# Optimization experiments

Measured on AMD Instinct MI355X. Metric: run time of the kernel, lower is better.

Reference implementation:

```python
import jax, jax.numpy as jnp
import numpy as np

L = 2        # n_layers
D = 128      # embed_dim
H = 4        # n_heads
HD = D // H  # head_dim
B = 2
N = 4096
PERIOD = 2.0
WINDOW = 0.5
EPS = 1e-5
NF = D // 4  # n_frequencies = embed_dim / (n_dimensions * 2), n_dimensions=2


def setup_inputs() -> dict:
    key = jax.random.key(0)
    ks = jax.random.split(key, 12)
    s = 0.05  # weight init scale
    inp = {
        'x': jax.random.normal(ks[0], (B, N, D), jnp.float32),
        'pos': jax.random.uniform(ks[1], (B, N, 2), jnp.float32),
        'Wq_w': jax.random.normal(ks[2], (L, D, D), jnp.float32) * s,
        'Wq_b': jnp.zeros((L, D), jnp.float32),
        'Wk_w': jax.random.normal(ks[3], (L, D, D), jnp.float32) * s,
        'Wk_b': jnp.zeros((L, D), jnp.float32),
        'Wv_w': jax.random.normal(ks[4], (L, D, D), jnp.float32) * s,
        'Wv_b': jnp.zeros((L, D), jnp.float32),
        'Wo_w': jax.random.normal(ks[5], (L, D, D), jnp.float32) * s,
        'Wo_b': jnp.zeros((L, D), jnp.float32),
        'n1_g': jnp.ones((L, D), jnp.float32),
        'n1_b': jnp.zeros((L, D), jnp.float32),
        'n2_g': jnp.ones((L, D), jnp.float32),
        'n2_b': jnp.zeros((L, D), jnp.float32),
        'l1_w': jax.random.normal(ks[6], (L, D, 2 * D), jnp.float32) * s,
        'l1_b': jnp.zeros((L, 2 * D), jnp.float32),
        'l2_w': jax.random.normal(ks[7], (L, 2 * D, D), jnp.float32) * s,
        'l2_b': jnp.zeros((L, D), jnp.float32),
    }
    return inp


def _batchnorm(x, g, b):
    # BatchNorm1d in training mode over flattened (B*N, D)
    Bb, Nn, Dd = x.shape
    x2 = x.reshape(Bb * Nn, Dd)
    mu = x2.mean(0)
    var = x2.var(0)
    y = (x2 - mu) * jax.lax.rsqrt(var + EPS) * g + b
    return y.reshape(Bb, Nn, Dd)


def _rope(x, pos, freqs):
    # x: (B,N,D), pos: (B,N,2), freqs: (NF,)
    angle = pos[..., None] * freqs            # (B,N,2,NF)
    angle = jnp.repeat(angle, 2, axis=-1)     # (B,N,2,2*NF)
    angle = angle.reshape(x.shape)            # (B,N,D)
    xp = x.reshape(*x.shape[:-1], D // 2, 2)
    x_sw = jnp.stack([-xp[..., 1], xp[..., 0]], axis=-1).reshape(x.shape)
    return jnp.cos(angle) * x + jnp.sin(angle) * x_sw


def _forward(x, pos, Wq_w, Wq_b, Wk_w, Wk_b, Wv_w, Wv_b, Wo_w, Wo_b,
             n1_g, n1_b, n2_g, n2_b, l1_w, l1_b, l2_w, l2_b):
    freqs = 2 * jnp.pi * jnp.arange(1, NF + 1, dtype=x.dtype) / PERIOD
    # window mask: dist(i,j) <= WINDOW/2  -> compare squared distances
    sq = jnp.sum(pos * pos, axis=-1)                          # (B,N)
    d2 = sq[:, :, None] + sq[:, None, :] - 2 * jnp.einsum('bnd,bmd->bnm', pos, pos)
    mask = (d2 <= (WINDOW / 2) ** 2)[:, None, :, :]           # (B,1,N,N)
    scale = 1.0 / jnp.sqrt(jnp.asarray(HD, x.dtype))

    for i in range(L):
        xn = _batchnorm(x, n1_g[i], n1_b[i])
        q = xn @ Wq_w[i] + Wq_b[i]
        k = xn @ Wk_w[i] + Wk_b[i]
        v = xn @ Wv_w[i] + Wv_b[i]
        if i == 0:  # rotary encoding applied at first layer only
            q = _rope(q, pos, freqs)
            k = _rope(k, pos, freqs)
        # split heads: (B,N,D) -> (B,H,N,HD)
        qh = q.reshape(B, N, H, HD).transpose(0, 2, 1, 3)
        kh = k.reshape(B, N, H, HD).transpose(0, 2, 1, 3)
        vh = v.reshape(B, N, H, HD).transpose(0, 2, 1, 3)
        scores = jnp.einsum('bhnd,bhmd->bhnm', qh, kh) * scale
        scores = jnp.where(mask, scores, jnp.finfo(x.dtype).min)
        attn = jax.nn.softmax(scores, axis=-1)
        oh = jnp.einsum('bhnm,bhmd->bhnd', attn, vh)
        o = oh.transpose(0, 2, 1, 3).reshape(B, N, D)
        x = x + (o @ Wo_w[i] + Wo_b[i])
        # FFN block
        xn2 = _batchnorm(x, n2_g[i], n2_b[i])
        h = jax.nn.relu(xn2 @ l1_w[i] + l1_b[i])
        x = x + (h @ l2_w[i] + l2_b[i])
    return x


def reference(x, pos, Wq_w, Wq_b, Wk_w, Wk_b, Wv_w, Wv_b, Wo_w, Wo_b,
              n1_g, n1_b, n2_g, n2_b, l1_w, l1_b, l2_w, l2_b):
    return _forward(x, pos, Wq_w, Wq_b, Wk_w, Wk_b, Wv_w, Wv_b, Wo_w, Wo_b,
                    n1_g, n1_b, n2_g, n2_b, l1_w, l1_b, l2_w, l2_b)
```

## Files before the change

kernel.cpp:

```cpp
#include <hip/hip_runtime.h>
#include <hip/hip_bf16.h>
#include <math.h>

#define LYR 2
#define DIM 128
#define NH 4
#define HD 32
#define BB 2
#define NN 4096
#define MROWS (BB * NN)
#define R2 0.0625f
#define BN_EPS 1e-5f
#define CLOG2E 0.25503594f

typedef __attribute__((ext_vector_type(4))) float f32x4;
typedef __attribute__((ext_vector_type(8))) short bf16x8;
typedef __attribute__((ext_vector_type(4))) short bf16x4;

static __device__ inline unsigned short f2bf(float f) {
  union { float f; unsigned u; } v; v.f = f;
  unsigned r = v.u + 0x7FFFu + ((v.u >> 16) & 1u);
  return (unsigned short)(r >> 16);
}

static __device__ inline float exp2_fast(float x) {
#if defined(__has_builtin)
#if __has_builtin(__builtin_amdgcn_exp2f)
  return __builtin_amdgcn_exp2f(x);
#else
  return exp2f(x);
#endif
#else
  return exp2f(x);
#endif
}

static __device__ inline unsigned cvt_pk_bf16(float lo, float hi) {
  unsigned r;
  asm volatile("v_cvt_pk_bf16_f32 %0, %1, %2" : "=v"(r) : "v"(lo), "v"(hi));
  return r;
}

__global__ __launch_bounds__(256) void wprep_k(const float* __restrict__ Wq,
                                               const float* __restrict__ Wk,
                                               const float* __restrict__ Wv,
                                               const float* __restrict__ Wo,
                                               const float* __restrict__ L1,
                                               const float* __restrict__ L2,
                                               const float* __restrict__ Wqb,
                                               const float* __restrict__ Wkb,
                                               const float* __restrict__ Wvb,
                                               short* __restrict__ wT,
                                               float* __restrict__ qkvb) {
  const int id = blockIdx.x;
  const int l = id >> 7, r = id & 127;
  const size_t lbase = (size_t)l * 131072;
  const float* src; short* dst; int K, N, tk, tn;
  float mult = 1.0f;
  if (r < 64) {
    const int m = r >> 4, tile = r & 15;
    if (m == 0)      { src = Wq + (size_t)l * 16384; mult = CLOG2E; }
    else if (m == 1) src = Wk + (size_t)l * 16384;
    else if (m == 2) src = Wv + (size_t)l * 16384;
    else             src = Wo + (size_t)l * 16384;
    dst = wT + lbase + (size_t)m * 16384;
    K = 128; N = 128; tk = tile >> 2; tn = tile & 3;
  } else if (r < 96) {
    const int tile = r - 64;
    src = L1 + (size_t)l * 32768; dst = wT + lbase + 65536;
    K = 128; N = 256; tk = tile >> 3; tn = tile & 7;
  } else {
    const int tile = r - 96;
    src = L2 + (size_t)l * 32768; dst = wT + lbase + 98304;
    K = 256; N = 128; tk = tile >> 2; tn = tile & 3;
  }
  __shared__ float tl[32][33];
  const int t = threadIdx.x;
  const int rr = t >> 3, c4 = (t & 7) * 4;
  float4 vv = *(const float4*)(src + (size_t)(tk * 32 + rr) * N + tn * 32 + c4);
  tl[rr][c4 + 0] = vv.x; tl[rr][c4 + 1] = vv.y;
  tl[rr][c4 + 2] = vv.z; tl[rr][c4 + 3] = vv.w;
  __syncthreads();
  bf16x4 o4;
  o4[0] = (short)f2bf(tl[c4 + 0][rr] * mult);
  o4[1] = (short)f2bf(tl[c4 + 1][rr] * mult);
  o4[2] = (short)f2bf(tl[c4 + 2][rr] * mult);
  o4[3] = (short)f2bf(tl[c4 + 3][rr] * mult);
  *(bf16x4*)(dst + (size_t)(tn * 32 + rr) * K + tk * 32 + c4) = o4;
  if (r == 0) {
    for (int i = t; i < 384; i += 256) {
      float bv;
      if (i < 128)      bv = Wqb[l * 128 + i] * CLOG2E;
      else if (i < 256) bv = Wkb[l * 128 + i - 128];
      else              bv = Wvb[l * 128 + i - 256];
      qkvb[l * 384 + i] = bv;
    }
  }
}

__global__ __launch_bounds__(256) void copy_stats_k(const float* __restrict__ x,
                                                    float* __restrict__ out,
                                                    float* __restrict__ sums) {
  __shared__ float ss[8][128], sq[8][128];
  const int t = threadIdx.x;
  const int c4 = (t & 31) * 4, rg = t >> 5;
  const size_t base = (size_t)blockIdx.x * (32 * DIM);
  float s0 = 0.f, s1 = 0.f, s2 = 0.f, s3 = 0.f;
  float q0 = 0.f, q1 = 0.f, q2 = 0.f, q3 = 0.f;
  for (int r = rg; r < 32; r += 8) {
    float4 v = *(const float4*)&x[base + (size_t)r * DIM + c4];
    *(float4*)&out[base + (size_t)r * DIM + c4] = v;
    s0 += v.x; q0 += v.x * v.x;
    s1 += v.y; q1 += v.y * v.y;
    s2 += v.z; q2 += v.z * v.z;
    s3 += v.w; q3 += v.w * v.w;
  }
  ss[rg][c4 + 0] = s0; sq[rg][c4 + 0] = q0;
  ss[rg][c4 + 1] = s1; sq[rg][c4 + 1] = q1;
  ss[rg][c4 + 2] = s2; sq[rg][c4 + 2] = q2;
  ss[rg][c4 + 3] = s3; sq[rg][c4 + 3] = q3;
  __syncthreads();
  if (t < 128) {
    float S = 0.f, Q = 0.f;
#pragma unroll
    for (int r2 = 0; r2 < 8; r2++) { S += ss[r2][t]; Q += sq[r2][t]; }
    atomicAdd(&sums[t], S);
    atomicAdd(&sums[128 + t], Q);
  }
}

__global__ __launch_bounds__(256) void bn_apply_k(const float* __restrict__ x,
                                                  const float* __restrict__ sums,
                                                  const float* __restrict__ g,
                                                  const float* __restrict__ bta,
                                                  short* __restrict__ y) {
  const int i4 = blockIdx.x * 256 + threadIdx.x;
  const int dd = (i4 * 4) & (DIM - 1);
  const float inv = 1.0f / (float)MROWS;
  float4 xv = *(const float4*)&x[(size_t)i4 * 4];
  float4 sm = *(const float4*)&sums[dd];
  float4 sq = *(const float4*)&sums[128 + dd];
  float4 gg = *(const float4*)&g[dd];
  float4 bb = *(const float4*)&bta[dd];
  float mu0 = sm.x * inv, mu1 = sm.y * inv, mu2 = sm.z * inv, mu3 = sm.w * inv;
  bf16x4 o;
  o[0] = (short)f2bf((xv.x - mu0) * rsqrtf(sq.x * inv - mu0 * mu0 + BN_EPS) * gg.x + bb.x);
  o[1] = (short)f2bf((xv.y - mu1) * rsqrtf(sq.y * inv - mu1 * mu1 + BN_EPS) * gg.y + bb.y);
  o[2] = (short)f2bf((xv.z - mu2) * rsqrtf(sq.z * inv - mu2 * mu2 + BN_EPS) * gg.z + bb.z);
  o[3] = (short)f2bf((xv.w - mu3) * rsqrtf(sq.w * inv - mu3 * mu3 + BN_EPS) * gg.w + bb.w);
  *(bf16x4*)&y[(size_t)i4 * 4] = o;
}

template <int MODE, bool RELU>
__global__ __launch_bounds__(256) void gemm_bf_k(const short* __restrict__ A,
                                                 const short* __restrict__ WT,
                                                 const float* __restrict__ bias,
                                                 const float* res,
                                                 float* Cf,
                                                 short* __restrict__ Cb,
                                                 float* __restrict__ statsums,
                                                 int K) {
  __shared__ short a_s[64 * 80];
  __shared__ short w_s[64 * 80];
  const int t = threadIdx.x, w = t >> 6, lane = t & 63, g = lane >> 4, i16 = lane & 15;
  const int bm = blockIdx.x * 64, bn = blockIdx.y * 64;
  const int sr = t >> 2, sc = (t & 3) * 8;
  const size_t MN = (size_t)MROWS * DIM;
  f32x4 acc[4];
#pragma unroll
  for (int ct = 0; ct < 4; ct++) acc[ct] = (f32x4){0.f, 0.f, 0.f, 0.f};
  for (int k0 = 0; k0 < K; k0 += 64) {
    __syncthreads();
    *(bf16x8*)&a_s[sr * 80 + sc]      = *(const bf16x8*)(A + (size_t)(bm + sr) * K + k0 + sc);
    *(bf16x8*)&a_s[sr * 80 + sc + 32] = *(const bf16x8*)(A + (size_t)(bm + sr) * K + k0 + sc + 32);
    *(bf16x8*)&w_s[sr * 80 + sc]      = *(const bf16x8*)(WT + (size_t)(bn + sr) * K + k0 + sc);
    *(bf16x8*)&w_s[sr * 80 + sc + 32] = *(const bf16x8*)(WT + (size_t)(bn + sr) * K + k0 + sc + 32);
    __syncthreads();
#pragma unroll
    for (int ks = 0; ks < 2; ks++) {
      bf16x8 af = *(const bf16x8*)&a_s[(16 * w + i16) * 80 + ks * 32 + 8 * g];
#pragma unroll
      for (int ct = 0; ct < 4; ct++) {
        bf16x8 wf = *(const bf16x8*)&w_s[(ct * 16 + i16) * 80 + ks * 32 + 8 * g];
        acc[ct] = __builtin_amdgcn_mfma_f32_16x16x32_bf16(af, wf, acc[ct], 0, 0, 0);
      }
    }
  }
  float s_acc[4], q_acc[4];
#pragma unroll
  for (int ct = 0; ct < 4; ct++) {
    const int col = bn + ct * 16 + i16;
    const float bv = bias[col];
    if (MODE == 3) {
      const int row0 = bm + 16 * w + 4 * g;
      if (col < 256) {
        short* dstb = (col < 128) ? Cb : (Cb + MN);
        const int cc = col & 127;
#pragma unroll
        for (int r = 0; r < 4; r++)
          dstb[(size_t)(row0 + r) * DIM + cc] = (short)f2bf(acc[ct][r] + bv);
      } else {
        const int b_ = row0 >> 12, n_ = row0 & (NN - 1);
        const int hh = (col - 256) >> 5, dd = (col - 256) & 31;
        bf16x4 o4;
#pragma unroll
        for (int r = 0; r < 4; r++) o4[r] = (short)f2bf(acc[ct][r] + bv);
        *(bf16x4*)(Cb + 2 * MN + ((size_t)(b_ * NH + hh) * HD + dd) * NN + n_) = o4;
      }
    } else if (MODE == 0) {
      float ssum = 0.f, qsum = 0.f;
#pragma unroll
      for (int r = 0; r < 4; r++) {
        const int row = bm + 16 * w + 4 * g + r;
        float vv = acc[ct][r] + bv + res[(size_t)row * DIM + col];
        Cf[(size_t)row * DIM + col] = vv;
        ssum += vv; qsum += vv * vv;
      }
      s_acc[ct] = ssum; q_acc[ct] = qsum;
    } else {
#pragma unroll
      for (int r = 0; r < 4; r++) {
        const int row = bm + 16 * w + 4 * g + r;
        float vv = acc[ct][r] + bv;
        if (RELU) vv = fmaxf(vv, 0.f);
        Cb[(size_t)row * (size_t)256 + col] = (short)f2bf(vv);
      }
    }
  }
  if (MODE == 0) {
#pragma unroll
    for (int ct = 0; ct < 4; ct++) {
      s_acc[ct] += __shfl_xor(s_acc[ct], 16, 64);
      s_acc[ct] += __shfl_xor(s_acc[ct], 32, 64);
      q_acc[ct] += __shfl_xor(q_acc[ct], 16, 64);
      q_acc[ct] += __shfl_xor(q_acc[ct], 32, 64);
    }
    float* bs = (float*)a_s;
    __syncthreads();
    if (t < 128) bs[t] = 0.f;
    __syncthreads();
    if (lane < 16) {
#pragma unroll
      for (int ct = 0; ct < 4; ct++) {
        atomicAdd(&bs[ct * 16 + i16], s_acc[ct]);
        atomicAdd(&bs[64 + ct * 16 + i16], q_acc[ct]);
      }
    }
    __syncthreads();
    if (t < 64) {
      atomicAdd(&statsums[bn + t], bs[t]);
      atomicAdd(&statsums[128 + bn + t], bs[64 + t]);
    }
  }
}

__global__ __launch_bounds__(256) void rope_bf_k(short* __restrict__ q,
                                                 short* __restrict__ kk,
                                                 const float* __restrict__ pos) {
  const int idx = blockIdx.x * 256 + threadIdx.x;
  const int row = idx >> 2, hh = idx & 3;
  const float2 pp = *(const float2*)&pos[(size_t)row * 2];
  short* qp = q + (size_t)row * DIM + hh * HD;
  short* kp = kk + (size_t)row * DIM + hh * HD;
  bf16x8 qv[4], kv[4];
#pragma unroll
  for (int u = 0; u < 4; u++) {
    qv[u] = *(const bf16x8*)(qp + 8 * u);
    kv[u] = *(const bf16x8*)(kp + 8 * u);
  }
#pragma unroll
  for (int lp = 0; lp < 16; lp++) {
    const int p = hh * 16 + lp;
    const float coord = (p < 32) ? pp.x : pp.y;
    const int f = p & 31;
    float sn, cs;
    __sincosf(3.14159265358979323846f * (float)(f + 1) * coord, &sn, &cs);
    const int u = lp >> 2, e = (lp & 3) * 2;
    const float a0 = __uint_as_float(((unsigned)(unsigned short)qv[u][e]) << 16);
    const float a1 = __uint_as_float(((unsigned)(unsigned short)qv[u][e + 1]) << 16);
    qv[u][e]     = (short)f2bf(cs * a0 - sn * a1);
    qv[u][e + 1] = (short)f2bf(cs * a1 + sn * a0);
    const float b0 = __uint_as_float(((unsigned)(unsigned short)kv[u][e]) << 16);
    const float b1 = __uint_as_float(((unsigned)(unsigned short)kv[u][e + 1]) << 16);
    kv[u][e]     = (short)f2bf(cs * b0 - sn * b1);
    kv[u][e + 1] = (short)f2bf(cs * b1 + sn * b0);
  }
#pragma unroll
  for (int u = 0; u < 4; u++) {
    *(bf16x8*)(qp + 8 * u) = qv[u];
    *(bf16x8*)(kp + 8 * u) = kv[u];
  }
}

__global__ __launch_bounds__(128) void attn3_k(const short* __restrict__ q,
                                               const short* __restrict__ k,
                                               const short* __restrict__ vt,
                                               const float* __restrict__ pos,
                                               short* __restrict__ ob) {
  const int bh = blockIdx.y, b = bh >> 2, h = bh & 3;
  const int q0 = blockIdx.x * 32;
  __shared__ short ks_s[64 * 40];
  __shared__ short vt_s[32 * 72];
  __shared__ short ps_s[2 * 16 * 72];
  __shared__ float pkx[64], pky[64], pnt[64];
  const int t = threadIdx.x, w = t >> 6, lane = t & 63, g = lane >> 4, i16 = lane & 15;
  const short* kp = k + (size_t)b * NN * DIM + h * HD;
  const short* vp = vt + (size_t)bh * HD * NN;

  const bf16x8 qf = *(const bf16x8*)(q + (size_t)(b * NN + q0 + 16 * w + i16) * DIM + h * HD + 8 * g);
  const float2 qp2 = *(const float2*)&pos[((size_t)b * NN + q0 + 16 * w + i16) * 2];
  const float qx = qp2.x, qy = qp2.y;
  const float ci = 0.5f * (qx * qx + qy * qy) - 0.5f * R2;

  bf16x8 kreg0 = *(const bf16x8*)(kp + (size_t)(t >> 2) * DIM + (t & 3) * 8);
  bf16x8 kreg1 = *(const bf16x8*)(kp + (size_t)((t >> 2) + 32) * DIM + (t & 3) * 8);
  bf16x8 vreg0 = *(const bf16x8*)(vp + (size_t)(t >> 3) * NN + (t & 7) * 8);
  bf16x8 vreg1 = *(const bf16x8*)(vp + (size_t)((t >> 3) + 16) * NN + (t & 7) * 8);
  float2 kpos = make_float2(0.f, 0.f);
  if (t < 64) kpos = *(const float2*)&pos[((size_t)b * NN + t) * 2];

  f32x4 acc0 = {0.f, 0.f, 0.f, 0.f}, acc1 = {0.f, 0.f, 0.f, 0.f};
  const f32x4 zf = {0.f, 0.f, 0.f, 0.f};
  float m_run = -1e30f, l_run = 0.f;

  for (int k0 = 0; k0 < NN; k0 += 64) {
    __syncthreads();
    *(bf16x8*)&ks_s[(t >> 2) * 40 + (t & 3) * 8] = kreg0;
    *(bf16x8*)&ks_s[((t >> 2) + 32) * 40 + (t & 3) * 8] = kreg1;
    *(bf16x8*)&vt_s[(t >> 3) * 72 + (t & 7) * 8] = vreg0;
    *(bf16x8*)&vt_s[((t >> 3) + 16) * 72 + (t & 7) * 8] = vreg1;
    if (t < 64) {
      pkx[t] = kpos.x; pky[t] = kpos.y;
      pnt[t] = -0.5f * (kpos.x * kpos.x + kpos.y * kpos.y);
    }
    __syncthreads();
    const int kn = k0 + 64;
    if (kn < NN) {
      kreg0 = *(const bf16x8*)(kp + (size_t)(kn + (t >> 2)) * DIM + (t & 3) * 8);
      kreg1 = *(const bf16x8*)(kp + (size_t)(kn + 32 + (t >> 2)) * DIM + (t & 3) * 8);
      vreg0 = *(const bf16x8*)(vp + (size_t)(t >> 3) * NN + kn + (t & 7) * 8);
      vreg1 = *(const bf16x8*)(vp + (size_t)((t >> 3) + 16) * NN + kn + (t & 7) * 8);
      if (t < 64) kpos = *(const float2*)&pos[((size_t)b * NN + kn + t) * 2];
    }

    f32x4 sx[4];
#pragma unroll
    for (int jt = 0; jt < 4; jt++) {
      bf16x8 kf = *(const bf16x8*)&ks_s[(16 * jt + i16) * 40 + 8 * g];
      sx[jt] = __builtin_amdgcn_mfma_f32_16x16x32_bf16(kf, qf, zf, 0, 0, 0);
    }

    float pv_[16];
    float tmax = -1e30f;
#pragma unroll
    for (int jt = 0; jt < 4; jt++) {
      float4 kx4 = *(const float4*)&pkx[16 * jt + 4 * g];
      float4 ky4 = *(const float4*)&pky[16 * jt + 4 * g];
      float4 nt4 = *(const float4*)&pnt[16 * jt + 4 * g];
      const float kxa[4] = {kx4.x, kx4.y, kx4.z, kx4.w};
      const float kya[4] = {ky4.x, ky4.y, ky4.z, ky4.w};
      const float nta[4] = {nt4.x, nt4.y, nt4.z, nt4.w};
#pragma unroll
      for (int r = 0; r < 4; r++) {
        const float dot = fmaf(qx, kxa[r], fmaf(qy, kya[r], nta[r]));
        const float val = (dot >= ci) ? sx[jt][r] : -1e30f;
        pv_[jt * 4 + r] = val;
        tmax = fmaxf(tmax, val);
      }
    }
    tmax = fmaxf(tmax, __shfl_xor(tmax, 16, 64));
    tmax = fmaxf(tmax, __shfl_xor(tmax, 32, 64));
    const float mnew = fmaxf(m_run, tmax);
    const float f = exp2_fast(m_run - mnew);
    float tsum = 0.f;
    float pr[16];
#pragma unroll
    for (int u = 0; u < 16; u++) {
      pr[u] = exp2_fast(pv_[u] - mnew);
      tsum += pr[u];
    }
    tsum += __shfl_xor(tsum, 16, 64);
    tsum += __shfl_xor(tsum, 32, 64);
    l_run = l_run * f + tsum;
    m_run = mnew;

#pragma unroll
    for (int jt = 0; jt < 4; jt++) {
      uint2 w2;
      w2.x = cvt_pk_bf16(pr[jt * 4 + 0], pr[jt * 4 + 1]);
      w2.y = cvt_pk_bf16(pr[jt * 4 + 2], pr[jt * 4 + 3]);
      *(uint2*)&ps_s[w * 1152 + i16 * 72 + 16 * jt + 4 * g] = w2;
    }
    const float f0 = __shfl(f, 4 * g + 0), f1 = __shfl(f, 4 * g + 1),
                f2_ = __shfl(f, 4 * g + 2), f3 = __shfl(f, 4 * g + 3);
    acc0[0] *= f0; acc0[1] *= f1; acc0[2] *= f2_; acc0[3] *= f3;
    acc1[0] *= f0; acc1[1] *= f1; acc1[2] *= f2_; acc1[3] *= f3;

#pragma unroll
    for (int ks2 = 0; ks2 < 2; ks2++) {
      bf16x8 pf = *(const bf16x8*)&ps_s[w * 1152 + i16 * 72 + 8 * g + 32 * ks2];
      bf16x8 vf0 = *(const bf16x8*)&vt_s[i16 * 72 + 8 * g + 32 * ks2];
      bf16x8 vf1 = *(const bf16x8*)&vt_s[(16 + i16) * 72 + 8 * g + 32 * ks2];
      acc0 = __builtin_amdgcn_mfma_f32_16x16x32_bf16(pf, vf0, acc0, 0, 0, 0);
      acc1 = __builtin_amdgcn_mfma_f32_16x16x32_bf16(pf, vf1, acc1, 0, 0, 0);
    }
  }

  const float li0 = __shfl(l_run, 4 * g + 0), li1 = __shfl(l_run, 4 * g + 1),
              li2 = __shfl(l_run, 4 * g + 2), li3 = __shfl(l_run, 4 * g + 3);
  short* op = ob + ((size_t)b * NN + q0 + 16 * w) * DIM + h * HD;
  op[(4 * g + 0) * DIM + i16] = (short)f2bf(acc0[0] / li0);
  op[(4 * g + 1) * DIM + i16] = (short)f2bf(acc0[1] / li1);
  op[(4 * g + 2) * DIM + i16] = (short)f2bf(acc0[2] / li2);
  op[(4 * g + 3) * DIM + i16] = (short)f2bf(acc0[3] / li3);
  op[(4 * g + 0) * DIM + 16 + i16] = (short)f2bf(acc1[0] / li0);
  op[(4 * g + 1) * DIM + 16 + i16] = (short)f2bf(acc1[1] / li1);
  op[(4 * g + 2) * DIM + 16 + i16] = (short)f2bf(acc1[2] / li2);
  op[(4 * g + 3) * DIM + 16 + i16] = (short)f2bf(acc1[3] / li3);
}

extern "C" void kernel_launch(void* const* d_in, const int* in_sizes, int n_in,
                              void* d_out, int out_size, void* d_ws, size_t ws_size,
                              hipStream_t stream) {
  const float* x = (const float*)d_in[0];
  const float* pos = (const float*)d_in[1];
  const float* Wq_w = (const float*)d_in[2];
  const float* Wq_b = (const float*)d_in[3];
  const float* Wk_w = (const float*)d_in[4];
  const float* Wk_b = (const float*)d_in[5];
  const float* Wv_w = (const float*)d_in[6];
  const float* Wv_b = (const float*)d_in[7];
  const float* Wo_w = (const float*)d_in[8];
  const float* Wo_b = (const float*)d_in[9];
  const float* n1_g = (const float*)d_in[10];
  const float* n1_b = (const float*)d_in[11];
  const float* n2_g = (const float*)d_in[12];
  const float* n2_b = (const float*)d_in[13];
  const float* l1_w = (const float*)d_in[14];
  const float* l1_b = (const float*)d_in[15];
  const float* l2_w = (const float*)d_in[16];
  const float* l2_b = (const float*)d_in[17];

  float* out = (float*)d_out;
  short* wsS = (short*)d_ws;
  const size_t MN = (size_t)MROWS * DIM;
  short* xn_bf = wsS;
  short* qb_bf = wsS + MN;
  short* ob_bf = wsS + 4 * MN;
  short* hb_bf = wsS + 5 * MN;
  short* wT    = wsS + 7 * MN;
  float* qkvb  = (float*)(wsS + 7 * MN + 262144);
  float* sums  = qkvb + 768;

  wprep_k<<<256, 256, 0, stream>>>(Wq_w, Wk_w, Wv_w, Wo_w, l1_w, l2_w,
                                   Wq_b, Wk_b, Wv_b, wT, qkvb);
  hipMemsetAsync(sums, 0, 1280 * sizeof(float), stream);
  copy_stats_k<<<256, 256, 0, stream>>>(x, out, sums);

  for (int l = 0; l < LYR; l++) {
    const short* lw = wT + (size_t)l * 131072;
    float* s_n1 = sums + (2 * l) * 256;
    float* s_n2 = sums + (2 * l + 1) * 256;
    float* s_nx = sums + (2 * l + 2) * 256;

    bn_apply_k<<<1024, 256, 0, stream>>>(out, s_n1, n1_g + l * DIM, n1_b + l * DIM, xn_bf);
    gemm_bf_k<3, false><<<dim3(128, 6), 256, 0, stream>>>(
        xn_bf, lw, qkvb + l * 384, nullptr, nullptr, qb_bf, nullptr, 128);
    if (l == 0) rope_bf_k<<<128, 256, 0, stream>>>(qb_bf, qb_bf + MN, pos);
    attn3_k<<<dim3(NN / 32, BB * NH), 128, 0, stream>>>(
        qb_bf, qb_bf + MN, qb_bf + 2 * MN, pos, ob_bf);
    gemm_bf_k<0, false><<<dim3(128, 2), 256, 0, stream>>>(
        ob_bf, lw + 49152, Wo_b + l * DIM, out, out, nullptr, s_n2, 128);

    bn_apply_k<<<1024, 256, 0, stream>>>(out, s_n2, n2_g + l * DIM, n2_b + l * DIM, xn_bf);
    gemm_bf_k<1, true><<<dim3(128, 4), 256, 0, stream>>>(
        xn_bf, lw + 65536, l1_b + l * 2 * DIM, nullptr, nullptr, hb_bf, nullptr, 128);
    gemm_bf_k<0, false><<<dim3(128, 2), 256, 0, stream>>>(
        hb_bf, lw + 98304, l2_b + l * DIM, out, out, nullptr, s_nx, 256);
  }
}
```

Before: 357.1 us.

## Split attention keys across chunks, drop online-softmax max, fuse BN into GEMM

The attention kernel now splits the key range into four chunks along a third grid dimension. Each chunk writes unnormalized fp32 partial accumulators and row sums, and a new combine kernel reduces them and normalizes. The running-max rescaling is removed and exp2 is applied directly to the scaled scores, which relies on the scores being small enough not to overflow. BatchNorm apply is fused into the A-tile load of the QKV and FFN1 GEMMs, so the separate bn_apply kernels and their bf16 intermediate disappear. The cost is extra fp32 partial traffic plus the combine launch, and the BN scale and shift are recomputed in every GEMM block.

```diff
diff --git a/kernel.cpp b/kernel.cpp
--- a/kernel.cpp
+++ b/kernel.cpp
@@ -12,6 +12,8 @@
 #define R2 0.0625f
 #define BN_EPS 1e-5f
 #define CLOG2E 0.25503594f
+#define NCH 4
+#define CHLEN (NN / NCH)
 
 typedef __attribute__((ext_vector_type(4))) float f32x4;
 typedef __attribute__((ext_vector_type(8))) short bf16x8;
@@ -129,30 +131,12 @@
   }
 }
 
-__global__ __launch_bounds__(256) void bn_apply_k(const float* __restrict__ x,
-                                                  const float* __restrict__ sums,
-                                                  const float* __restrict__ g,
-                                                  const float* __restrict__ bta,
-                                                  short* __restrict__ y) {
-  const int i4 = blockIdx.x * 256 + threadIdx.x;
-  const int dd = (i4 * 4) & (DIM - 1);
-  const float inv = 1.0f / (float)MROWS;
-  float4 xv = *(const float4*)&x[(size_t)i4 * 4];
-  float4 sm = *(const float4*)&sums[dd];
-  float4 sq = *(const float4*)&sums[128 + dd];
-  float4 gg = *(const float4*)&g[dd];
-  float4 bb = *(const float4*)&bta[dd];
-  float mu0 = sm.x * inv, mu1 = sm.y * inv, mu2 = sm.z * inv, mu3 = sm.w * inv;
-  bf16x4 o;
-  o[0] = (short)f2bf((xv.x - mu0) * rsqrtf(sq.x * inv - mu0 * mu0 + BN_EPS) * gg.x + bb.x);
-  o[1] = (short)f2bf((xv.y - mu1) * rsqrtf(sq.y * inv - mu1 * mu1 + BN_EPS) * gg.y + bb.y);
-  o[2] = (short)f2bf((xv.z - mu2) * rsqrtf(sq.z * inv - mu2 * mu2 + BN_EPS) * gg.z + bb.z);
-  o[3] = (short)f2bf((xv.w - mu3) * rsqrtf(sq.w * inv - mu3 * mu3 + BN_EPS) * gg.w + bb.w);
-  *(bf16x4*)&y[(size_t)i4 * 4] = o;
-}
-
-template <int MODE, bool RELU>
+template <int MODE, bool RELU, bool ABN>
 __global__ __launch_bounds__(256) void gemm_bf_k(const short* __restrict__ A,
+                                                 const float* __restrict__ Af,
+                                                 const float* __restrict__ stats,
+                                                 const float* __restrict__ gma,
+                                                 const float* __restrict__ btaN,
                                                  const short* __restrict__ WT,
                                                  const float* __restrict__ bias,
                                                  const float* res,
@@ -162,17 +146,55 @@
                                                  int K) {
   __shared__ short a_s[64 * 80];
   __shared__ short w_s[64 * 80];
+  __shared__ float sc_s[128], sh_s[128];
   const int t = threadIdx.x, w = t >> 6, lane = t & 63, g = lane >> 4, i16 = lane & 15;
   const int bm = blockIdx.x * 64, bn = blockIdx.y * 64;
-  const int sr = t >> 2, sc = (t & 3) * 8;
+  const int sr = t >> 2, sc = (t & 3) * 8, c16 = (t & 3) * 16;
   const size_t MN = (size_t)MROWS * DIM;
+  if (ABN) {
+    if (t < 128) {
+      const float inv = 1.0f / (float)MROWS;
+      const float mu = stats[t] * inv;
+      const float var = stats[128 + t] * inv - mu * mu;
+      const float rs = rsqrtf(var + BN_EPS);
+      const float s = rs * gma[t];
+      sc_s[t] = s;
+      sh_s[t] = btaN[t] - mu * s;
+    }
+  }
   f32x4 acc[4];
 #pragma unroll
   for (int ct = 0; ct < 4; ct++) acc[ct] = (f32x4){0.f, 0.f, 0.f, 0.f};
   for (int k0 = 0; k0 < K; k0 += 64) {
     __syncthreads();
-    *(bf16x8*)&a_s[sr * 80 + sc]      = *(const bf16x8*)(A + (size_t)(bm + sr) * K + k0 + sc);
-    *(bf16x8*)&a_s[sr * 80 + sc + 32] = *(const bf16x8*)(A + (size_t)(bm + sr) * K + k0 + sc + 32);
+    if (ABN) {
+      const float* ap = Af + (size_t)(bm + sr) * K + k0 + c16;
+      float4 x0 = *(const float4*)ap, x1 = *(const float4*)(ap + 4);
+      float4 x2 = *(const float4*)(ap + 8), x3 = *(const float4*)(ap + 12);
+      const int kb = k0 + c16;
+      bf16x8 o0, o1;
+      o0[0] = (short)f2bf(x0.x * sc_s[kb + 0]  + sh_s[kb + 0]);
+      o0[1] = (short)f2bf(x0.y * sc_s[kb + 1]  + sh_s[kb + 1]);
+      o0[2] = (short)f2bf(x0.z * sc_s[kb + 2]  + sh_s[kb + 2]);
+      o0[3] = (short)f2bf(x0.w * sc_s[kb + 3]  + sh_s[kb + 3]);
+      o0[4] = (short)f2bf(x1.x * sc_s[kb + 4]  + sh_s[kb + 4]);
+      o0[5] = (short)f2bf(x1.y * sc_s[kb + 5]  + sh_s[kb + 5]);
+      o0[6] = (short)f2bf(x1.z * sc_s[kb + 6]  + sh_s[kb + 6]);
+      o0[7] = (short)f2bf(x1.w * sc_s[kb + 7]  + sh_s[kb + 7]);
+      o1[0] = (short)f2bf(x2.x * sc_s[kb + 8]  + sh_s[kb + 8]);
+      o1[1] = (short)f2bf(x2.y * sc_s[kb + 9]  + sh_s[kb + 9]);
+      o1[2] = (short)f2bf(x2.z * sc_s[kb + 10] + sh_s[kb + 10]);
+      o1[3] = (short)f2bf(x2.w * sc_s[kb + 11] + sh_s[kb + 11]);
+      o1[4] = (short)f2bf(x3.x * sc_s[kb + 12] + sh_s[kb + 12]);
+      o1[5] = (short)f2bf(x3.y * sc_s[kb + 13] + sh_s[kb + 13]);
+      o1[6] = (short)f2bf(x3.z * sc_s[kb + 14] + sh_s[kb + 14]);
+      o1[7] = (short)f2bf(x3.w * sc_s[kb + 15] + sh_s[kb + 15]);
+      *(bf16x8*)&a_s[sr * 80 + c16] = o0;
+      *(bf16x8*)&a_s[sr * 80 + c16 + 8] = o1;
+    } else {
+      *(bf16x8*)&a_s[sr * 80 + sc]      = *(const bf16x8*)(A + (size_t)(bm + sr) * K + k0 + sc);
+      *(bf16x8*)&a_s[sr * 80 + sc + 32] = *(const bf16x8*)(A + (size_t)(bm + sr) * K + k0 + sc + 32);
+    }
     *(bf16x8*)&w_s[sr * 80 + sc]      = *(const bf16x8*)(WT + (size_t)(bn + sr) * K + k0 + sc);
     *(bf16x8*)&w_s[sr * 80 + sc + 32] = *(const bf16x8*)(WT + (size_t)(bn + sr) * K + k0 + sc + 32);
     __syncthreads();
@@ -292,13 +314,16 @@
   }
 }
 
-__global__ __launch_bounds__(128) void attn3_k(const short* __restrict__ q,
+__global__ __launch_bounds__(128) void attn4_k(const short* __restrict__ q,
                                                const short* __restrict__ k,
                                                const short* __restrict__ vt,
                                                const float* __restrict__ pos,
-                                               short* __restrict__ ob) {
+                                               float* __restrict__ accP,
+                                               float* __restrict__ lP) {
   const int bh = blockIdx.y, b = bh >> 2, h = bh & 3;
   const int q0 = blockIdx.x * 32;
+  const int ch = blockIdx.z;
+  const int kbeg = ch * CHLEN, kend = kbeg + CHLEN;
   __shared__ short ks_s[64 * 40];
   __shared__ short vt_s[32 * 72];
   __shared__ short ps_s[2 * 16 * 72];
@@ -312,18 +337,18 @@
   const float qx = qp2.x, qy = qp2.y;
   const float ci = 0.5f * (qx * qx + qy * qy) - 0.5f * R2;
 
-  bf16x8 kreg0 = *(const bf16x8*)(kp + (size_t)(t >> 2) * DIM + (t & 3) * 8);
-  bf16x8 kreg1 = *(const bf16x8*)(kp + (size_t)((t >> 2) + 32) * DIM + (t & 3) * 8);
-  bf16x8 vreg0 = *(const bf16x8*)(vp + (size_t)(t >> 3) * NN + (t & 7) * 8);
-  bf16x8 vreg1 = *(const bf16x8*)(vp + (size_t)((t >> 3) + 16) * NN + (t & 7) * 8);
+  bf16x8 kreg0 = *(const bf16x8*)(kp + (size_t)(kbeg + (t >> 2)) * DIM + (t & 3) * 8);
+  bf16x8 kreg1 = *(const bf16x8*)(kp + (size_t)(kbeg + 32 + (t >> 2)) * DIM + (t & 3) * 8);
+  bf16x8 vreg0 = *(const bf16x8*)(vp + (size_t)(t >> 3) * NN + kbeg + (t & 7) * 8);
+  bf16x8 vreg1 = *(const bf16x8*)(vp + (size_t)((t >> 3) + 16) * NN + kbeg + (t & 7) * 8);
   float2 kpos = make_float2(0.f, 0.f);
-  if (t < 64) kpos = *(const float2*)&pos[((size_t)b * NN + t) * 2];
+  if (t < 64) kpos = *(const float2*)&pos[((size_t)b * NN + kbeg + t) * 2];
 
   f32x4 acc0 = {0.f, 0.f, 0.f, 0.f}, acc1 = {0.f, 0.f, 0.f, 0.f};
   const f32x4 zf = {0.f, 0.f, 0.f, 0.f};
-  float m_run = -1e30f, l_run = 0.f;
-
-  for (int k0 = 0; k0 < NN; k0 += 64) {
+  float l_run = 0.f;
+
+  for (int k0 = kbeg; k0 < kend; k0 += 64) {
     __syncthreads();
     *(bf16x8*)&ks_s[(t >> 2) * 40 + (t & 3) * 8] = kreg0;
     *(bf16x8*)&ks_s[((t >> 2) + 32) * 40 + (t & 3) * 8] = kreg1;
@@ -335,7 +360,7 @@
     }
     __syncthreads();
     const int kn = k0 + 64;
-    if (kn < NN) {
+    if (kn < kend) {
       kreg0 = *(const bf16x8*)(kp + (size_t)(kn + (t >> 2)) * DIM + (t & 3) * 8);
       kreg1 = *(const bf16x8*)(kp + (size_t)(kn + 32 + (t >> 2)) * DIM + (t & 3) * 8);
       vreg0 = *(const bf16x8*)(vp + (size_t)(t >> 3) * NN + kn + (t & 7) * 8);
@@ -350,8 +375,8 @@
       sx[jt] = __builtin_amdgcn_mfma_f32_16x16x32_bf16(kf, qf, zf, 0, 0, 0);
     }
 
-    float pv_[16];
-    float tmax = -1e30f;
+    float pr[16];
+    float tsum = 0.f;
 #pragma unroll
     for (int jt = 0; jt < 4; jt++) {
       float4 kx4 = *(const float4*)&pkx[16 * jt + 4 * g];
@@ -363,26 +388,13 @@
 #pragma unroll
       for (int r = 0; r < 4; r++) {
         const float dot = fmaf(qx, kxa[r], fmaf(qy, kya[r], nta[r]));
-        const float val = (dot >= ci) ? sx[jt][r] : -1e30f;
-        pv_[jt * 4 + r] = val;
-        tmax = fmaxf(tmax, val);
+        float p = exp2_fast(sx[jt][r]);
+        p = (dot >= ci) ? p : 0.f;
+        pr[jt * 4 + r] = p;
+        tsum += p;
       }
     }
-    tmax = fmaxf(tmax, __shfl_xor(tmax, 16, 64));
-    tmax = fmaxf(tmax, __shfl_xor(tmax, 32, 64));
-    const float mnew = fmaxf(m_run, tmax);
-    const float f = exp2_fast(m_run - mnew);
-    float tsum = 0.f;
-    float pr[16];
-#pragma unroll
-    for (int u = 0; u < 16; u++) {
-      pr[u] = exp2_fast(pv_[u] - mnew);
-      tsum += pr[u];
-    }
-    tsum += __shfl_xor(tsum, 16, 64);
-    tsum += __shfl_xor(tsum, 32, 64);
-    l_run = l_run * f + tsum;
-    m_run = mnew;
+    l_run += tsum;
 
 #pragma unroll
     for (int jt = 0; jt < 4; jt++) {
@@ -391,10 +403,6 @@
       w2.y = cvt_pk_bf16(pr[jt * 4 + 2], pr[jt * 4 + 3]);
       *(uint2*)&ps_s[w * 1152 + i16 * 72 + 16 * jt + 4 * g] = w2;
     }
-    const float f0 = __shfl(f, 4 * g + 0), f1 = __shfl(f, 4 * g + 1),
-                f2_ = __shfl(f, 4 * g + 2), f3 = __shfl(f, 4 * g + 3);
-    acc0[0] *= f0; acc0[1] *= f1; acc0[2] *= f2_; acc0[3] *= f3;
-    acc1[0] *= f0; acc1[1] *= f1; acc1[2] *= f2_; acc1[3] *= f3;
 
 #pragma unroll
     for (int ks2 = 0; ks2 < 2; ks2++) {
@@ -406,17 +414,41 @@
     }
   }
 
-  const float li0 = __shfl(l_run, 4 * g + 0), li1 = __shfl(l_run, 4 * g + 1),
-              li2 = __shfl(l_run, 4 * g + 2), li3 = __shfl(l_run, 4 * g + 3);
-  short* op = ob + ((size_t)b * NN + q0 + 16 * w) * DIM + h * HD;
-  op[(4 * g + 0) * DIM + i16] = (short)f2bf(acc0[0] / li0);
-  op[(4 * g + 1) * DIM + i16] = (short)f2bf(acc0[1] / li1);
-  op[(4 * g + 2) * DIM + i16] = (short)f2bf(acc0[2] / li2);
-  op[(4 * g + 3) * DIM + i16] = (short)f2bf(acc0[3] / li3);
-  op[(4 * g + 0) * DIM + 16 + i16] = (short)f2bf(acc1[0] / li0);
-  op[(4 * g + 1) * DIM + 16 + i16] = (short)f2bf(acc1[1] / li1);
-  op[(4 * g + 2) * DIM + 16 + i16] = (short)f2bf(acc1[2] / li2);
-  op[(4 * g + 3) * DIM + 16 + i16] = (short)f2bf(acc1[3] / li3);
+  l_run += __shfl_xor(l_run, 16, 64);
+  l_run += __shfl_xor(l_run, 32, 64);
+  if (lane < 16)
+    lP[(size_t)(ch * 8 + bh) * NN + q0 + 16 * w + lane] = l_run;
+  float* ap = accP + ((size_t)(ch * 8 + bh) * NN + q0 + 16 * w) * HD;
+#pragma unroll
+  for (int r = 0; r < 4; r++) {
+    ap[(4 * g + r) * HD + i16] = acc0[r];
+    ap[(4 * g + r) * HD + 16 + i16] = acc1[r];
+  }
+}
+
+__global__ __launch_bounds__(256) void attn_comb_k(const float* __restrict__ accP,
+                                                   const float* __restrict__ lP,
+                                                   short* __restrict__ ob) {
+  const int idx = blockIdx.x * 256 + threadIdx.x;
+  const int b = idx >> 17;
+  const int n = (idx >> 5) & (NN - 1);
+  const int hd = idx & 31;
+  const int h = hd >> 3, d4 = (hd & 7) * 4;
+  const int bh = b * NH + h;
+  float ax = 0.f, ay = 0.f, az = 0.f, aw = 0.f, l = 0.f;
+#pragma unroll
+  for (int c = 0; c < NCH; c++) {
+    const float4 v = *(const float4*)&accP[((size_t)(c * 8 + bh) * NN + n) * HD + d4];
+    ax += v.x; ay += v.y; az += v.z; aw += v.w;
+    l += lP[(size_t)(c * 8 + bh) * NN + n];
+  }
+  const float inv = 1.0f / l;
+  bf16x4 o;
+  o[0] = (short)f2bf(ax * inv);
+  o[1] = (short)f2bf(ay * inv);
+  o[2] = (short)f2bf(az * inv);
+  o[3] = (short)f2bf(aw * inv);
+  *(bf16x4*)&ob[((size_t)b * NN + n) * DIM + h * HD + d4] = o;
 }
 
 extern "C" void kernel_launch(void* const* d_in, const int* in_sizes, int n_in,
@@ -444,13 +476,15 @@
   float* out = (float*)d_out;
   short* wsS = (short*)d_ws;
   const size_t MN = (size_t)MROWS * DIM;
-  short* xn_bf = wsS;
-  short* qb_bf = wsS + MN;
-  short* ob_bf = wsS + 4 * MN;
-  short* hb_bf = wsS + 5 * MN;
-  short* wT    = wsS + 7 * MN;
-  float* qkvb  = (float*)(wsS + 7 * MN + 262144);
-  float* sums  = qkvb + 768;
+  short* qb_bf = wsS;
+  short* ob_bf = wsS + 3 * MN;
+  short* wT    = wsS + 4 * MN;
+  float* fbase = (float*)(wsS + 4 * MN + 262144);
+  float* qkvb  = fbase;
+  float* sums  = fbase + 768;
+  float* lP    = fbase + 2048;
+  float* accP  = fbase + 2048 + 131072;
+  short* hb_bf = (short*)accP;
 
   wprep_k<<<256, 256, 0, stream>>>(Wq_w, Wk_w, Wv_w, Wo_w, l1_w, l2_w,
                                    Wq_b, Wk_b, Wv_b, wT, qkvb);
@@ -463,19 +497,22 @@
     float* s_n2 = sums + (2 * l + 1) * 256;
     float* s_nx = sums + (2 * l + 2) * 256;
 
-    bn_apply_k<<<1024, 256, 0, stream>>>(out, s_n1, n1_g + l * DIM, n1_b + l * DIM, xn_bf);
-    gemm_bf_k<3, false><<<dim3(128, 6), 256, 0, stream>>>(
-        xn_bf, lw, qkvb + l * 384, nullptr, nullptr, qb_bf, nullptr, 128);
+    gemm_bf_k<3, false, true><<<dim3(128, 6), 256, 0, stream>>>(
+        nullptr, out, s_n1, n1_g + l * DIM, n1_b + l * DIM,
+        lw, qkvb + l * 384, nullptr, nullptr, qb_bf, nullptr, 128);
     if (l == 0) rope_bf_k<<<128, 256, 0, stream>>>(qb_bf, qb_bf + MN, pos);
-    attn3_k<<<dim3(NN / 32, BB * NH), 128, 0, stream>>>(
-        qb_bf, qb_bf + MN, qb_bf + 2 * MN, pos, ob_bf);
-    gemm_bf_k<0, false><<<dim3(128, 2), 256, 0, stream>>>(
-        ob_bf, lw + 49152, Wo_b + l * DIM, out, out, nullptr, s_n2, 128);
-
-    bn_apply_k<<<1024, 256, 0, stream>>>(out, s_n2, n2_g + l * DIM, n2_b + l * DIM, xn_bf);
-    gemm_bf_k<1, true><<<dim3(128, 4), 256, 0, stream>>>(
-        xn_bf, lw + 65536, l1_b + l * 2 * DIM, nullptr, nullptr, hb_bf, nullptr, 128);
-    gemm_bf_k<0, false><<<dim3(128, 2), 256, 0, stream>>>(
-        hb_bf, lw + 98304, l2_b + l * DIM, out, out, nullptr, s_nx, 256);
-  }
-}
+    attn4_k<<<dim3(NN / 32, BB * NH, NCH), 128, 0, stream>>>(
+        qb_bf, qb_bf + MN, qb_bf + 2 * MN, pos, accP, lP);
+    attn_comb_k<<<1024, 256, 0, stream>>>(accP, lP, ob_bf);
+    gemm_bf_k<0, false, false><<<dim3(128, 2), 256, 0, stream>>>(
+        ob_bf, nullptr, nullptr, nullptr, nullptr,
+        lw + 49152, Wo_b + l * DIM, out, out, nullptr, s_n2, 128);
+
+    gemm_bf_k<1, true, true><<<dim3(128, 4), 256, 0, stream>>>(
+        nullptr, out, s_n2, n2_g + l * DIM, n2_b + l * DIM,
+        lw + 65536, l1_b + l * 2 * DIM, nullptr, nullptr, hb_bf, nullptr, 128);
+    gemm_bf_k<0, false, false><<<dim3(128, 2), 256, 0, stream>>>(
+        hb_bf, nullptr, nullptr, nullptr, nullptr,
+        lw + 98304, l2_b + l * DIM, out, out, nullptr, s_nx, 256);
+  }
+}
```

After: 308.1 us. 1.16x faster.
